# Kernel tuning notes

Measured on AMD Instinct MI355X. Metric: run time of the kernel, lower is better.

The kernel has to match this reference:

```python
import jax, jax.numpy as jnp
import numpy as np

LN_EPS = 1e-5


def setup_inputs() -> dict:
    key = jax.random.key(0)
    ks = jax.random.split(key, 4)
    B, D, N = 256, 1024, 100000
    scale = 1.0 / np.sqrt(D)
    return {
        "query": jax.random.normal(ks[0], (B, D), dtype=jnp.float32),
        "W1": jax.random.normal(ks[1], (D, D), dtype=jnp.float32) * scale,
        "b1": jnp.zeros((D,), dtype=jnp.float32),
        "ln_g": jnp.ones((D,), dtype=jnp.float32),
        "ln_b": jnp.zeros((D,), dtype=jnp.float32),
        "W2": jax.random.normal(ks[2], (D, D), dtype=jnp.float32) * scale,
        "b2": jnp.zeros((D,), dtype=jnp.float32),
        "memory": jax.random.normal(ks[3], (N, D), dtype=jnp.float32),
        "k": 16,
    }


def _l2norm(x):
    # F.normalize(p=2, dim=-1): x / max(||x||, eps) with eps=1e-12
    n = jnp.sqrt(jnp.sum(x * x, axis=-1, keepdims=True))
    return x / jnp.maximum(n, 1e-12)


def _layernorm(x, g, b):
    mu = jnp.mean(x, axis=-1, keepdims=True)
    var = jnp.mean((x - mu) ** 2, axis=-1, keepdims=True)
    return (x - mu) * jax.lax.rsqrt(var + LN_EPS) * g + b


def reference(query, W1, b1, ln_g, ln_b, W2, b2, memory, k):
    # project(): Linear -> LayerNorm -> GELU (exact) -> Linear -> L2 normalize
    h = query @ W1.T + b1                      # [B, D]
    h = _layernorm(h, ln_g, ln_b)
    h = jax.nn.gelu(h, approximate=False)
    refined = _l2norm(h @ W2.T + b2)           # [B, D]

    # retrieve_similar(): cosine sims against normalized memory bank, then top-k
    mem_n = _l2norm(memory)                    # [N, D]
    sims = refined @ mem_n.T                   # [B, N]
    topk_vals, topk_idx = jax.lax.top_k(sims, k)   # [B, k]
    retrieved = mem_n[topk_idx]                # [B, k, D] gather
    return refined, topk_vals, topk_idx, retrieved
```

## Files before the change

### kernel.cpp

```cpp
#include <hip/hip_runtime.h>
#include <float.h>
#include <math.h>

#define D 1024
#define BQ 256
#define NMEM 100000
#define TOPK 16
#define NT_TOT 1563

typedef __attribute__((ext_vector_type(4))) float f32x4;
typedef __attribute__((ext_vector_type(8))) short s16x8;

__device__ __forceinline__ void mfma16(f32x4& d, s16x8 a, s16x8 b) {
  asm("v_mfma_f32_16x16x32_bf16 %0, %1, %2, %0" : "+v"(d) : "v"(a), "v"(b));
}

typedef __attribute__((address_space(3))) unsigned int lds_u32_t;
typedef __attribute__((address_space(1))) const unsigned int gbl_u32_t;
__device__ __forceinline__ void async_copy16(const void* gsrc, void* ldst) {
  __builtin_amdgcn_global_load_lds((gbl_u32_t*)gsrc, (lds_u32_t*)ldst, 16, 0, 0);
}

#define GLOAD(dst, addr) \
  asm volatile("global_load_dwordx4 %0, %1, off" : "=v"(dst) : "v"(addr))

__device__ __forceinline__ unsigned short bf16rtne(float x) {
  unsigned u = __float_as_uint(x);
  unsigned r = u + 0x7fffu + ((u >> 16) & 1u);
  return (unsigned short)(r >> 16);
}

__device__ __forceinline__ void cvt8(f32x4 a, f32x4 b, s16x8* hi, s16x8* lo,
                                     float* ssq) {
  float xs[8] = {a[0], a[1], a[2], a[3], b[0], b[1], b[2], b[3]};
  union { s16x8 v; unsigned short u[8]; } H, L;
#pragma unroll
  for (int e = 0; e < 8; ++e) {
    float x = xs[e];
    unsigned short h = bf16rtne(x);
    float hf = __uint_as_float(((unsigned)h) << 16);
    H.u[e] = (short)h;
    L.u[e] = (short)bf16rtne(x - hf);
    *ssq = fmaf(x, x, *ssq);
  }
  *hi = H.v;
  *lo = L.v;
}


__device__ __forceinline__ float waveReduceSum(float v) {
#pragma unroll
  for (int o = 32; o > 0; o >>= 1) v += __shfl_xor(v, o, 64);
  return v;
}

__device__ __forceinline__ float blockReduceSum(float v, float* sbuf) {
  v = waveReduceSum(v);
  int w = threadIdx.x >> 6;
  if ((threadIdx.x & 63) == 0) sbuf[w] = v;
  __syncthreads();
  float r = sbuf[0] + sbuf[1] + sbuf[2] + sbuf[3];
  __syncthreads();
  return r;
}


__global__ __launch_bounds__(256) void prep_bf16_kernel(
    const float* __restrict__ src, float* __restrict__ dst, int R16) {
  int g = blockIdx.x * 256 + threadIdx.x;
  int l = g & 63;
  int mt = (g >> 6) % R16;
  int kb = (g >> 6) / R16;
  int row = mt * 16 + (l & 15);
  int k0 = kb * 32 + ((l >> 4) << 3);
  const float* s = src + (size_t)row * D + k0;
  float4 v0 = *(const float4*)s;
  float4 v1 = *(const float4*)(s + 4);
  float xs[8] = {v0.x, v0.y, v0.z, v0.w, v1.x, v1.y, v1.z, v1.w};
  union { uint4 q; unsigned short u[8]; } H, L;
#pragma unroll
  for (int e = 0; e < 8; ++e) {
    float x = xs[e];
    unsigned short h = bf16rtne(x);
    float hf = __uint_as_float(((unsigned)h) << 16);
    H.u[e] = h;
    L.u[e] = bf16rtne(x - hf);
  }
  char* db = (char*)dst + (size_t)kb * (R16 * 2048) + mt * 2048 + l * 16;
  *(uint4*)db = H.q;
  *(uint4*)(db + 1024) = L.q;
}


__global__ __launch_bounds__(256) void mfma_gemm_kernel(
    const float* __restrict__ Afr, const float* __restrict__ Wfr,
    float* __restrict__ part) {
  int t = threadIdx.x;
  int w = t >> 6, l = t & 63;
  int ct = blockIdx.x & 63;
  int kc = blockIdx.x >> 6;
  f32x4 acc[4];
  f32x4 zz = {0.f, 0.f, 0.f, 0.f};
#pragma unroll
  for (int mi = 0; mi < 4; ++mi) acc[mi] = zz;
  const char* ab0 = (const char*)Afr + w * 8192 + l * 16;
  const char* bb0 = (const char*)Wfr + ct * 2048 + l * 16;
#pragma unroll 2
  for (int s = 0; s < 8; ++s) {
    int kb = kc * 8 + s;
    const char* bb = bb0 + (size_t)kb * 131072;
    s16x8 bh = *(const s16x8*)(bb);
    s16x8 bl = *(const s16x8*)(bb + 1024);
    const char* ab = ab0 + (size_t)kb * 32768;
#pragma unroll
    for (int mi = 0; mi < 4; ++mi) {
      s16x8 ah = *(const s16x8*)(ab + mi * 2048);
      s16x8 al = *(const s16x8*)(ab + mi * 2048 + 1024);
      mfma16(acc[mi], ah, bh);
      mfma16(acc[mi], ah, bl);
      mfma16(acc[mi], al, bh);
    }
  }
  float* pb = part + (size_t)kc * 262144 + ct * 16 + (l & 15);
#pragma unroll
  for (int mi = 0; mi < 4; ++mi)
#pragma unroll
    for (int j = 0; j < 4; ++j) {
      int row = w * 64 + mi * 16 + ((l >> 4) << 2) + j;
      pb[(size_t)row * 1024] = acc[mi][j];
    }
}


__global__ __launch_bounds__(256) void reduce_ln_gelu_kernel(
    const float* __restrict__ part, const float* __restrict__ bias,
    const float* __restrict__ g, const float* __restrict__ b,
    float* __restrict__ Hf) {
  __shared__ float sbuf[4];
  int row = blockIdx.x, t = threadIdx.x;
  const float* p = part + (size_t)row * 1024 + t * 4;
  float4 x0 = *(const float4*)(p);
  float4 x1 = *(const float4*)(p + 262144);
  float4 x2 = *(const float4*)(p + 524288);
  float4 x3 = *(const float4*)(p + 786432);
  float4 bb = *(const float4*)(bias + t * 4);
  float vx = x0.x + x1.x + x2.x + x3.x + bb.x;
  float vy = x0.y + x1.y + x2.y + x3.y + bb.y;
  float vz = x0.z + x1.z + x2.z + x3.z + bb.z;
  float vw = x0.w + x1.w + x2.w + x3.w + bb.w;
  float s = blockReduceSum(vx + vy + vz + vw, sbuf);
  float mu = s * (1.0f / D);
  float dx = vx - mu, dy = vy - mu, dz = vz - mu, dw = vw - mu;
  float ss = blockReduceSum(dx * dx + dy * dy + dz * dz + dw * dw, sbuf);
  float rstd = rsqrtf(ss * (1.0f / D) + 1e-5f);
  float4 gg = *(const float4*)(g + t * 4);
  float4 be = *(const float4*)(b + t * 4);
  float y[4];
  y[0] = dx * rstd * gg.x + be.x;
  y[1] = dy * rstd * gg.y + be.y;
  y[2] = dz * rstd * gg.z + be.z;
  y[3] = dw * rstd * gg.w + be.w;
  const float c = 0.70710678118654752f;
  union { uint2 q; unsigned short u[4]; } H, L;
#pragma unroll
  for (int e = 0; e < 4; ++e) {
    float ye = 0.5f * y[e] * (1.0f + erff(y[e] * c));
    unsigned short h = bf16rtne(ye);
    float hf = __uint_as_float(((unsigned)h) << 16);
    H.u[e] = h;
    L.u[e] = bf16rtne(ye - hf);
  }
  int kb = t >> 3, oct = (t >> 1) & 3;
  char* db = (char*)Hf + (size_t)kb * 32768 + (row >> 4) * 2048 +
             ((row & 15) + oct * 16) * 16 + (t & 1) * 8;
  *(uint2*)db = H.q;
  *(uint2*)(db + 1024) = L.q;
}


__global__ __launch_bounds__(256) void reduce_l2norm_kernel(
    const float* __restrict__ part, const float* __restrict__ bias,
    float* __restrict__ outRef, float* __restrict__ Af) {
  __shared__ float sbuf[4];
  int row = blockIdx.x, t = threadIdx.x;
  const float* p = part + (size_t)row * 1024 + t * 4;
  float4 x0 = *(const float4*)(p);
  float4 x1 = *(const float4*)(p + 262144);
  float4 x2 = *(const float4*)(p + 524288);
  float4 x3 = *(const float4*)(p + 786432);
  float4 bb = *(const float4*)(bias + t * 4);
  float vx = x0.x + x1.x + x2.x + x3.x + bb.x;
  float vy = x0.y + x1.y + x2.y + x3.y + bb.y;
  float vz = x0.z + x1.z + x2.z + x3.z + bb.z;
  float vw = x0.w + x1.w + x2.w + x3.w + bb.w;
  float ss = blockReduceSum(vx * vx + vy * vy + vz * vz + vw * vw, sbuf);
  float inv = 1.0f / fmaxf(sqrtf(ss), 1e-12f);
  float y[4] = {vx * inv, vy * inv, vz * inv, vw * inv};
  *(float4*)(outRef + (size_t)row * D + t * 4) =
      make_float4(y[0], y[1], y[2], y[3]);
  union { uint2 q; unsigned short u[4]; } H, L;
#pragma unroll
  for (int e = 0; e < 4; ++e) {
    unsigned short h = bf16rtne(y[e]);
    float hf = __uint_as_float(((unsigned)h) << 16);
    H.u[e] = h;
    L.u[e] = bf16rtne(y[e] - hf);
  }
  int kb = t >> 3, oct = (t >> 1) & 3;
  char* db = (char*)Af + (size_t)kb * 32768 + (row >> 4) * 2048 +
             ((row & 15) + oct * 16) * 16 + (t & 1) * 8;
  *(uint2*)db = H.q;
  *(uint2*)(db + 1024) = L.q;
}

__global__ void zero_ctrs_kernel(int* c) { c[threadIdx.x] = 0; }


#define SBODY(J, CV0, CV1, NV0, NV1, PBR, PBW, DO_A, DO_PF, DO_CONV, VMC,      \
              DO_BAR2, VME)                                                    \
  do {                                                                         \
    _Pragma("unroll") for (int mi = 0; mi < 4; ++mi) {                         \
      const char* ab_ = smem + (w4 + mi) * 2048 + l * 16;                      \
      ah[mi] = *(const s16x8*)ab_;                                             \
      al[mi] = *(const s16x8*)(ab_ + 1024);                                    \
    }                                                                          \
    asm volatile("s_waitcnt lgkmcnt(0)\n\ts_barrier" ::: "memory");            \
    if (DO_A) {                                                                \
      const char* as_ =                                                        \
          afbytes + (size_t)((J) + 1) * 32768 + w * 8192 + l * 16;             \
      char* ad_ = smem + w * 8192;                                             \
      _Pragma("unroll") for (int u = 0; u < 8; ++u)                            \
        async_copy16(as_ + u * 1024, ad_ + u * 1024);                          \
    }                                                                          \
    if (DO_PF) {                                                               \
      const float* p_ = bsrc + ((J) + 2) * 32;                                 \
      GLOAD(NV0, p_);                                                          \
      GLOAD(NV1, p_ + 4);                                                      \
    }                                                                          \
    if (DO_CONV) {                                                             \
      asm volatile("s_waitcnt vmcnt(" #VMC ")" ::: "memory");                  \
      __builtin_amdgcn_sched_barrier(0);                                       \
      s16x8 bhn_, bln_;                                                        \
      cvt8(CV0, CV1, &bhn_, &bln_, &ssq);                                      \
      *(s16x8*)(smem + 32768 + (PBW)*8192 + bwoff) = bhn_;                     \
      *(s16x8*)(smem + 32768 + (PBW)*8192 + bwoff + 1024) = bln_;              \
    }                                                                          \
    __builtin_amdgcn_s_setprio(1);                                             \
    _Pragma("unroll") for (int ni = 0; ni < 4; ++ni) {                         \
      const char* bb_ = smem + 32768 + (PBR)*8192 + ni * 2048 + l * 16;        \
      s16x8 bh_ = *(const s16x8*)bb_;                                          \
      s16x8 bl_ = *(const s16x8*)(bb_ + 1024);                                 \
      _Pragma("unroll") for (int mi = 0; mi < 4; ++mi) {                       \
        mfma16(acc[mi][ni], ah[mi], bh_);                                      \
        mfma16(acc[mi][ni], ah[mi], bl_);                                      \
        mfma16(acc[mi][ni], al[mi], bh_);                                      \
      }                                                                        \
    }                                                                          \
    __builtin_amdgcn_s_setprio(0);                                             \
    if (DO_BAR2)                                                               \
      asm volatile("s_waitcnt vmcnt(" #VME ") lgkmcnt(0)\n\ts_barrier" :::     \
                       "memory");                                              \
  } while (0)

__global__ __launch_bounds__(256, 3) void sims_gemm_kernel(
    const float* __restrict__ Afrag, const float* __restrict__ mem,
    float* __restrict__ invn, int* __restrict__ ctr,
    float* __restrict__ simsbuf, int ntiles, int chunk_n0, int stride_cols) {
  __shared__ __align__(16) char smem[50432];
  __shared__ int s_tile;
  const int t = threadIdx.x;
  const int w = t >> 6, l = t & 63;
  const int w4 = w * 4;
  const int brow_loc = t >> 2;
  const int kseg = t & 3;
  const int bwoff = (brow_loc >> 4) * 2048 + ((brow_loc & 15) + kseg * 16) * 16;
  const char* afbytes = (const char*)Afrag;
  float* sPf = (float*)(smem + 49152);
  float* sInvF = (float*)(smem + 50176);

  while (true) {
    if (t == 0) s_tile = atomicAdd(ctr, 1);
    __syncthreads();
    const int unit = s_tile;
    if (unit >= ntiles) break;
    const int n0 = chunk_n0 + unit * 64;
    const int brow = min(n0 + brow_loc, NMEM - 1);
    const float* bsrc = mem + (size_t)brow * D + kseg * 8;

    f32x4 acc[4][4];
    f32x4 zz = {0.f, 0.f, 0.f, 0.f};
#pragma unroll
    for (int mi = 0; mi < 4; ++mi)
#pragma unroll
      for (int ni = 0; ni < 4; ++ni) acc[mi][ni] = zz;
    float ssq = 0.f;
    s16x8 ah[4], al[4];
    f32x4 br_a0, br_a1, br_b0, br_b1;

    GLOAD(br_a0, bsrc);
    GLOAD(br_a1, bsrc + 4);
    {
      const float* p1 = bsrc + 32;
      GLOAD(br_b0, p1);
      GLOAD(br_b1, p1 + 4);
    }
    {
      const char* as_ = afbytes + w * 8192 + l * 16;
      char* ad_ = smem + w * 8192;
#pragma unroll
      for (int u = 0; u < 8; ++u) async_copy16(as_ + u * 1024, ad_ + u * 1024);
    }
    asm volatile("s_waitcnt vmcnt(10)" ::: "memory");
    __builtin_amdgcn_sched_barrier(0);
    {
      s16x8 bh0, bl0;
      cvt8(br_a0, br_a1, &bh0, &bl0, &ssq);
      *(s16x8*)(smem + 32768 + bwoff) = bh0;
      *(s16x8*)(smem + 32768 + bwoff + 1024) = bl0;
    }
    asm volatile("s_waitcnt vmcnt(2) lgkmcnt(0)\n\ts_barrier" ::: "memory");

#pragma unroll 1
    for (int j = 0; j < 30; j += 2) {
      SBODY(j, br_b0, br_b1, br_a0, br_a1, 0, 1, 1, 1, 1, 10, 1, 2);
      SBODY(j + 1, br_a0, br_a1, br_b0, br_b1, 1, 0, 1, 1, 1, 10, 1, 2);
    }
    SBODY(30, br_b0, br_b1, br_a0, br_a1, 0, 1, 1, 0, 1, 8, 1, 0);
    SBODY(31, br_a0, br_a1, br_b0, br_b1, 1, 0, 0, 0, 0, 0, 0, 0);

    __syncthreads();
    sPf[t] = ssq;
    __syncthreads();
    if (t < 64) {
      float s = sPf[t * 4] + sPf[t * 4 + 1] + sPf[t * 4 + 2] + sPf[t * 4 + 3];
      float inv = 1.0f / fmaxf(sqrtf(s), 1e-12f);
      sInvF[t] = inv;
      int col = n0 + t;
      if (col < NMEM) invn[col] = inv;
    }
    __syncthreads();
    float siv[4];
#pragma unroll
    for (int ni = 0; ni < 4; ++ni) siv[ni] = sInvF[ni * 16 + (l & 15)];
    float* srow = simsbuf + (size_t)(unit * 64);
#pragma unroll
    for (int mi = 0; mi < 4; ++mi)
#pragma unroll
      for (int jj = 0; jj < 4; ++jj) {
        int row = w * 64 + mi * 16 + ((l >> 4) << 2) + jj;
        float* rp = srow + (size_t)row * stride_cols;
#pragma unroll
        for (int ni = 0; ni < 4; ++ni)
          rp[ni * 16 + (l & 15)] = acc[mi][ni][jj] * siv[ni];
      }
  }
}


__global__ __launch_bounds__(512) void topk_chunk_kernel(
    const float* __restrict__ simsbuf, int stride_cols, int chunk_n0,
    int nvalid, float* __restrict__ cv, int* __restrict__ ci) {
  __shared__ float wvv[8];
  __shared__ int wii[8];
  __shared__ float sbv;
  __shared__ int sbi;
  int row = blockIdx.x, t = threadIdx.x;
  const float* S = simsbuf + (size_t)row * stride_cols;
  float tv[16];
  int ti[16];
#pragma unroll
  for (int s = 0; s < 16; ++s) { tv[s] = -FLT_MAX; ti[s] = 2147483647; }
  float curMin = -FLT_MAX;
  for (int c0 = t * 4; c0 < nvalid; c0 += 2048) {
    float vv[4] = {-FLT_MAX, -FLT_MAX, -FLT_MAX, -FLT_MAX};
    if (c0 + 4 <= nvalid) {
      float4 v = *(const float4*)(S + c0);
      vv[0] = v.x; vv[1] = v.y; vv[2] = v.z; vv[3] = v.w;
    } else {
#pragma unroll
      for (int e = 0; e < 4; ++e)
        if (c0 + e < nvalid) vv[e] = S[c0 + e];
    }
#pragma unroll
    for (int e = 0; e < 4; ++e) {
      float v = vv[e];
      if (v > curMin) {
        int n = chunk_n0 + c0 + e;
        int ms = 0;
        float mv = tv[0];
#pragma unroll
        for (int s = 1; s < 16; ++s)
          if (tv[s] < mv) { mv = tv[s]; ms = s; }
#pragma unroll
        for (int s = 0; s < 16; ++s)
          if (s == ms) { tv[s] = v; ti[s] = n; }
        curMin = tv[0];
#pragma unroll
        for (int s = 1; s < 16; ++s) curMin = fminf(curMin, tv[s]);
      }
    }
  }
  float lastV = FLT_MAX;
  int lastI = -1;
  for (int pass = 0; pass < TOPK; ++pass) {
    float bv = -FLT_MAX;
    int bi = 2147483647;
#pragma unroll
    for (int s = 0; s < 16; ++s) {
      float v = tv[s];
      int idx = ti[s];
      bool qual = (v < lastV) || (v == lastV && idx > lastI);
      bool bet = (v > bv) || (v == bv && idx < bi);
      if (qual && bet) { bv = v; bi = idx; }
    }
#pragma unroll
    for (int o = 32; o > 0; o >>= 1) {
      float v2 = __shfl_xor(bv, o, 64);
      int i2 = __shfl_xor(bi, o, 64);
      if (v2 > bv || (v2 == bv && i2 < bi)) { bv = v2; bi = i2; }
    }
    if ((t & 63) == 0) { wvv[t >> 6] = bv; wii[t >> 6] = bi; }
    __syncthreads();
    if (t == 0) {
      float fv = wvv[0];
      int fi = wii[0];
#pragma unroll
      for (int u = 1; u < 8; ++u) {
        if (wvv[u] > fv || (wvv[u] == fv && wii[u] < fi)) {
          fv = wvv[u];
          fi = wii[u];
        }
      }
      sbv = fv;
      sbi = fi;
      cv[row * TOPK + pass] = fv;
      ci[row * TOPK + pass] = fi;
    }
    __syncthreads();
    lastV = sbv;
    lastI = sbi;
  }
}


__global__ __launch_bounds__(64) void final_merge_kernel(
    const float* __restrict__ cand_v, const int* __restrict__ cand_i,
    int nchunk, float* __restrict__ out_vals, float* __restrict__ out_idx) {
  int row = blockIdx.x, l = threadIdx.x;
  int nc = nchunk * TOPK;
  float mv[8];
  int mi_[8];
#pragma unroll
  for (int u = 0; u < 8; ++u) {
    int p = l + u * 64;
    if (p < nc) {
      int ch = p >> 4;
      mv[u] = cand_v[ch * 4096 + row * TOPK + (p & 15)];
      mi_[u] = cand_i[ch * 4096 + row * TOPK + (p & 15)];
    } else {
      mv[u] = -FLT_MAX;
      mi_[u] = 2147483647;
    }
  }
  float lastV = FLT_MAX;
  int lastI = -1;
  for (int pass = 0; pass < TOPK; ++pass) {
    float bv = -FLT_MAX;
    int bi = 2147483647;
#pragma unroll
    for (int u = 0; u < 8; ++u) {
      bool qual = (mv[u] < lastV) || (mv[u] == lastV && mi_[u] > lastI);
      bool bet = (mv[u] > bv) || (mv[u] == bv && mi_[u] < bi);
      if (qual && bet) { bv = mv[u]; bi = mi_[u]; }
    }
#pragma unroll
    for (int o = 32; o > 0; o >>= 1) {
      float v2 = __shfl_xor(bv, o, 64);
      int i2 = __shfl_xor(bi, o, 64);
      if (v2 > bv || (v2 == bv && i2 < bi)) { bv = v2; bi = i2; }
    }
    bv = __shfl(bv, 0, 64);
    bi = __shfl(bi, 0, 64);
    if (l == 0) {
      out_vals[row * TOPK + pass] = bv;
      out_idx[row * TOPK + pass] = (float)bi;
    }
    lastV = bv;
    lastI = bi;
  }
}


__global__ __launch_bounds__(256) void gather_kernel(
    const float* __restrict__ out_idx, const float* __restrict__ mem,
    const float* __restrict__ invn, float* __restrict__ out_retr) {
  int p = blockIdx.x;
  int idx = (int)out_idx[p];
  float inv = invn[idx];
  int c = threadIdx.x * 4;
  float4 v = *(const float4*)(mem + (size_t)idx * D + c);
  v.x *= inv; v.y *= inv; v.z *= inv; v.w *= inv;
  *(float4*)(out_retr + (size_t)p * D + c) = v;
}


extern "C" void kernel_launch(void* const* d_in, const int* in_sizes, int n_in,
                              void* d_out, int out_size, void* d_ws,
                              size_t ws_size, hipStream_t stream) {
  const float* query = (const float*)d_in[0];
  const float* W1 = (const float*)d_in[1];
  const float* b1 = (const float*)d_in[2];
  const float* ln_g = (const float*)d_in[3];
  const float* ln_b = (const float*)d_in[4];
  const float* W2 = (const float*)d_in[5];
  const float* b2 = (const float*)d_in[6];
  const float* mem = (const float*)d_in[7];

  float* out = (float*)d_out;
  float* out_refined = out;
  float* out_vals = out + 262144;
  float* out_idx = out + 262144 + 4096;
  float* out_retr = out + 262144 + 8192;

  float* wsp = (float*)d_ws;
  float* invn = wsp;
  float* Qf = wsp + 100352;
  float* Af = wsp + 362496;
  float* W1f = wsp + 624640;
  float* W2f = wsp + 1673216;
  float* part = wsp + 2721792;
  float* cand_v = wsp + 3770368;
  int* cand_i = (int*)(wsp + 3901440);
  int* ctrs = (int*)(wsp + 4032512);
  float* sims = wsp + 4032576;

  long ws_floats = (long)(ws_size / 4);
  long avail = ws_floats - 4032640;
  int tpc = (int)(avail / 16384);
  if (tpc > NT_TOT) tpc = NT_TOT;
  if (tpc < 1) tpc = 1;
  int nchunk = (NT_TOT + tpc - 1) / tpc;
  if (nchunk > 32) nchunk = 32;
  tpc = (NT_TOT + nchunk - 1) / nchunk;
  int stride = tpc * 64;

  zero_ctrs_kernel<<<1, 64, 0, stream>>>(ctrs);
  prep_bf16_kernel<<<128, 256, 0, stream>>>(query, Qf, 16);
  prep_bf16_kernel<<<512, 256, 0, stream>>>(W1, W1f, 64);
  prep_bf16_kernel<<<512, 256, 0, stream>>>(W2, W2f, 64);
  mfma_gemm_kernel<<<256, 256, 0, stream>>>(Qf, W1f, part);
  reduce_ln_gelu_kernel<<<256, 256, 0, stream>>>(part, b1, ln_g, ln_b, Qf);
  mfma_gemm_kernel<<<256, 256, 0, stream>>>(Qf, W2f, part);
  reduce_l2norm_kernel<<<256, 256, 0, stream>>>(part, b2, out_refined, Af);
  for (int c = 0; c < nchunk; ++c) {
    int t0 = c * tpc;
    int nt = NT_TOT - t0;
    if (nt > tpc) nt = tpc;
    if (nt <= 0) break;
    int base = t0 * 64;
    sims_gemm_kernel<<<768, 256, 0, stream>>>(Af, mem, invn, ctrs + c, sims,
                                              nt, base, stride);
    int nvalid = NMEM - base;
    if (nvalid > nt * 64) nvalid = nt * 64;
    topk_chunk_kernel<<<256, 512, 0, stream>>>(sims, stride, base, nvalid,
                                               cand_v + c * 4096,
                                               cand_i + c * 4096);
  }
  final_merge_kernel<<<256, 64, 0, stream>>>(cand_v, cand_i, nchunk, out_vals,
                                             out_idx);
  gather_kernel<<<BQ * TOPK, 256, 0, stream>>>(out_idx, mem, invn, out_retr);
}
```

Measured before the change: 419.7 us.

## Load A fragments directly to registers and triple-buffer B prefetch in sims GEMM

```diff
diff --git a/kernel.cpp b/kernel.cpp
--- a/kernel.cpp
+++ b/kernel.cpp
@@ -15,24 +15,15 @@
   asm("v_mfma_f32_16x16x32_bf16 %0, %1, %2, %0" : "+v"(d) : "v"(a), "v"(b));
 }
 
-typedef __attribute__((address_space(3))) unsigned int lds_u32_t;
-typedef __attribute__((address_space(1))) const unsigned int gbl_u32_t;
-__device__ __forceinline__ void async_copy16(const void* gsrc, void* ldst) {
-  __builtin_amdgcn_global_load_lds((gbl_u32_t*)gsrc, (lds_u32_t*)ldst, 16, 0, 0);
-}
-
-#define GLOAD(dst, addr) \
-  asm volatile("global_load_dwordx4 %0, %1, off" : "=v"(dst) : "v"(addr))
-
 __device__ __forceinline__ unsigned short bf16rtne(float x) {
   unsigned u = __float_as_uint(x);
   unsigned r = u + 0x7fffu + ((u >> 16) & 1u);
   return (unsigned short)(r >> 16);
 }
 
-__device__ __forceinline__ void cvt8(f32x4 a, f32x4 b, s16x8* hi, s16x8* lo,
+__device__ __forceinline__ void cvt8(float4 a, float4 b, s16x8* hi, s16x8* lo,
                                      float* ssq) {
-  float xs[8] = {a[0], a[1], a[2], a[3], b[0], b[1], b[2], b[3]};
+  float xs[8] = {a.x, a.y, a.z, a.w, b.x, b.y, b.z, b.w};
   union { s16x8 v; unsigned short u[8]; } H, L;
 #pragma unroll
   for (int e = 0; e < 8; ++e) {
@@ -216,72 +207,64 @@
 __global__ void zero_ctrs_kernel(int* c) { c[threadIdx.x] = 0; }
 
 
-#define SBODY(J, CV0, CV1, NV0, NV1, PBR, PBW, DO_A, DO_PF, DO_CONV, VMC,      \
-              DO_BAR2, VME)                                                    \
+#define SBODY(J, BP, ACh, ACl, ANh, ANl, RC0, RC1, RP0, RP1, DOPFB, DOPFA,    \
+              DOCONV)                                                          \
   do {                                                                         \
-    _Pragma("unroll") for (int mi = 0; mi < 4; ++mi) {                         \
-      const char* ab_ = smem + (w4 + mi) * 2048 + l * 16;                      \
-      ah[mi] = *(const s16x8*)ab_;                                             \
-      al[mi] = *(const s16x8*)(ab_ + 1024);                                    \
+    if (DOCONV) {                                                              \
+      s16x8 bhn_, bln_;                                                        \
+      cvt8(RC0, RC1, &bhn_, &bln_, &ssq);                                      \
+      char* bw_ = smem + (1 - (BP)) * 8192 + bwoff;                            \
+      *(s16x8*)bw_ = bhn_;                                                     \
+      *(s16x8*)(bw_ + 1024) = bln_;                                            \
     }                                                                          \
-    asm volatile("s_waitcnt lgkmcnt(0)\n\ts_barrier" ::: "memory");            \
-    if (DO_A) {                                                                \
-      const char* as_ =                                                        \
-          afbytes + (size_t)((J) + 1) * 32768 + w * 8192 + l * 16;             \
-      char* ad_ = smem + w * 8192;                                             \
-      _Pragma("unroll") for (int u = 0; u < 8; ++u)                            \
-        async_copy16(as_ + u * 1024, ad_ + u * 1024);                          \
+    if (DOPFA) {                                                               \
+      const char* an_ = afbytes + (size_t)((J) + 1) * 32768 + w4x + l * 16;    \
+      _Pragma("unroll") for (int mi = 0; mi < 4; ++mi) {                       \
+        ANh[mi] = *(const s16x8*)(an_ + mi * 2048);                            \
+        ANl[mi] = *(const s16x8*)(an_ + mi * 2048 + 1024);                     \
+      }                                                                        \
     }                                                                          \
-    if (DO_PF) {                                                               \
-      const float* p_ = bsrc + ((J) + 2) * 32;                                 \
-      GLOAD(NV0, p_);                                                          \
-      GLOAD(NV1, p_ + 4);                                                      \
-    }                                                                          \
-    if (DO_CONV) {                                                             \
-      asm volatile("s_waitcnt vmcnt(" #VMC ")" ::: "memory");                  \
-      __builtin_amdgcn_sched_barrier(0);                                       \
-      s16x8 bhn_, bln_;                                                        \
-      cvt8(CV0, CV1, &bhn_, &bln_, &ssq);                                      \
-      *(s16x8*)(smem + 32768 + (PBW)*8192 + bwoff) = bhn_;                     \
-      *(s16x8*)(smem + 32768 + (PBW)*8192 + bwoff + 1024) = bln_;              \
+    if (DOPFB) {                                                               \
+      const float* p_ = bsrc + ((J) + 3) * 32;                                 \
+      RP0 = *(const float4*)p_;                                                \
+      RP1 = *(const float4*)(p_ + 4);                                          \
     }                                                                          \
     __builtin_amdgcn_s_setprio(1);                                             \
     _Pragma("unroll") for (int ni = 0; ni < 4; ++ni) {                         \
-      const char* bb_ = smem + 32768 + (PBR)*8192 + ni * 2048 + l * 16;        \
+      const char* bb_ = smem + (BP)*8192 + ni * 2048 + l * 16;                 \
       s16x8 bh_ = *(const s16x8*)bb_;                                          \
       s16x8 bl_ = *(const s16x8*)(bb_ + 1024);                                 \
       _Pragma("unroll") for (int mi = 0; mi < 4; ++mi) {                       \
-        mfma16(acc[mi][ni], ah[mi], bh_);                                      \
-        mfma16(acc[mi][ni], ah[mi], bl_);                                      \
-        mfma16(acc[mi][ni], al[mi], bh_);                                      \
+        mfma16(acc[mi][ni], ACh[mi], bh_);                                     \
+        mfma16(acc[mi][ni], ACh[mi], bl_);                                     \
+        mfma16(acc[mi][ni], ACl[mi], bh_);                                     \
       }                                                                        \
     }                                                                          \
     __builtin_amdgcn_s_setprio(0);                                             \
-    if (DO_BAR2)                                                               \
-      asm volatile("s_waitcnt vmcnt(" #VME ") lgkmcnt(0)\n\ts_barrier" :::     \
-                       "memory");                                              \
+    asm volatile("s_waitcnt lgkmcnt(0)\n\ts_barrier" ::: "memory");            \
+    __builtin_amdgcn_sched_barrier(0);                                         \
   } while (0)
 
-__global__ __launch_bounds__(256, 3) void sims_gemm_kernel(
+__global__ __launch_bounds__(256, 2) void sims_gemm_kernel(
     const float* __restrict__ Afrag, const float* __restrict__ mem,
     float* __restrict__ invn, int* __restrict__ ctr,
     float* __restrict__ simsbuf, int ntiles, int chunk_n0, int stride_cols) {
-  __shared__ __align__(16) char smem[50432];
+  __shared__ __align__(16) char smem[16384];
+  __shared__ float sInvF[64];
   __shared__ int s_tile;
   const int t = threadIdx.x;
   const int w = t >> 6, l = t & 63;
-  const int w4 = w * 4;
+  const int w4x = (w * 4) * 2048;
   const int brow_loc = t >> 2;
   const int kseg = t & 3;
   const int bwoff = (brow_loc >> 4) * 2048 + ((brow_loc & 15) + kseg * 16) * 16;
   const char* afbytes = (const char*)Afrag;
-  float* sPf = (float*)(smem + 49152);
-  float* sInvF = (float*)(smem + 50176);
 
   while (true) {
     if (t == 0) s_tile = atomicAdd(ctr, 1);
     __syncthreads();
     const int unit = s_tile;
+    __syncthreads();
     if (unit >= ntiles) break;
     const int n0 = chunk_n0 + unit * 64;
     const int brow = min(n0 + brow_loc, NMEM - 1);
@@ -294,48 +277,57 @@
 #pragma unroll
       for (int ni = 0; ni < 4; ++ni) acc[mi][ni] = zz;
     float ssq = 0.f;
-    s16x8 ah[4], al[4];
-    f32x4 br_a0, br_a1, br_b0, br_b1;
-
-    GLOAD(br_a0, bsrc);
-    GLOAD(br_a1, bsrc + 4);
+
+    float4 r0a, r0b, r1a, r1b, r2a, r2b;
+    s16x8 s0h[4], s0l[4], s1h[4], s1l[4];
+
+    r0a = *(const float4*)bsrc;
+    r0b = *(const float4*)(bsrc + 4);
+    r1a = *(const float4*)(bsrc + 32);
+    r1b = *(const float4*)(bsrc + 36);
+    r2a = *(const float4*)(bsrc + 64);
+    r2b = *(const float4*)(bsrc + 68);
     {
-      const float* p1 = bsrc + 32;
-      GLOAD(br_b0, p1);
-      GLOAD(br_b1, p1 + 4);
-    }
-    {
-      const char* as_ = afbytes + w * 8192 + l * 16;
-      char* ad_ = smem + w * 8192;
-#pragma unroll
-      for (int u = 0; u < 8; ++u) async_copy16(as_ + u * 1024, ad_ + u * 1024);
-    }
-    asm volatile("s_waitcnt vmcnt(10)" ::: "memory");
-    __builtin_amdgcn_sched_barrier(0);
+      const char* a0_ = afbytes + w4x + l * 16;
+#pragma unroll
+      for (int mi = 0; mi < 4; ++mi) {
+        s0h[mi] = *(const s16x8*)(a0_ + mi * 2048);
+        s0l[mi] = *(const s16x8*)(a0_ + mi * 2048 + 1024);
+      }
+    }
     {
       s16x8 bh0, bl0;
-      cvt8(br_a0, br_a1, &bh0, &bl0, &ssq);
-      *(s16x8*)(smem + 32768 + bwoff) = bh0;
-      *(s16x8*)(smem + 32768 + bwoff + 1024) = bl0;
-    }
-    asm volatile("s_waitcnt vmcnt(2) lgkmcnt(0)\n\ts_barrier" ::: "memory");
+      cvt8(r0a, r0b, &bh0, &bl0, &ssq);
+      *(s16x8*)(smem + bwoff) = bh0;
+      *(s16x8*)(smem + bwoff + 1024) = bl0;
+    }
+    asm volatile("s_waitcnt lgkmcnt(0)\n\ts_barrier" ::: "memory");
+    __builtin_amdgcn_sched_barrier(0);
 
 #pragma unroll 1
-    for (int j = 0; j < 30; j += 2) {
-      SBODY(j, br_b0, br_b1, br_a0, br_a1, 0, 1, 1, 1, 1, 10, 1, 2);
-      SBODY(j + 1, br_a0, br_a1, br_b0, br_b1, 1, 0, 1, 1, 1, 10, 1, 2);
-    }
-    SBODY(30, br_b0, br_b1, br_a0, br_a1, 0, 1, 1, 0, 1, 8, 1, 0);
-    SBODY(31, br_a0, br_a1, br_b0, br_b1, 1, 0, 0, 0, 0, 0, 0, 0);
-
-    __syncthreads();
-    sPf[t] = ssq;
-    __syncthreads();
-    if (t < 64) {
-      float s = sPf[t * 4] + sPf[t * 4 + 1] + sPf[t * 4 + 2] + sPf[t * 4 + 3];
-      float inv = 1.0f / fmaxf(sqrtf(s), 1e-12f);
-      sInvF[t] = inv;
-      int col = n0 + t;
+    for (int jb = 0; jb < 24; jb += 6) {
+      SBODY(jb + 0, 0, s0h, s0l, s1h, s1l, r1a, r1b, r0a, r0b, 1, 1, 1);
+      SBODY(jb + 1, 1, s1h, s1l, s0h, s0l, r2a, r2b, r1a, r1b, 1, 1, 1);
+      SBODY(jb + 2, 0, s0h, s0l, s1h, s1l, r0a, r0b, r2a, r2b, 1, 1, 1);
+      SBODY(jb + 3, 1, s1h, s1l, s0h, s0l, r1a, r1b, r0a, r0b, 1, 1, 1);
+      SBODY(jb + 4, 0, s0h, s0l, s1h, s1l, r2a, r2b, r1a, r1b, 1, 1, 1);
+      SBODY(jb + 5, 1, s1h, s1l, s0h, s0l, r0a, r0b, r2a, r2b, 1, 1, 1);
+    }
+    SBODY(24, 0, s0h, s0l, s1h, s1l, r1a, r1b, r0a, r0b, 1, 1, 1);
+    SBODY(25, 1, s1h, s1l, s0h, s0l, r2a, r2b, r1a, r1b, 1, 1, 1);
+    SBODY(26, 0, s0h, s0l, s1h, s1l, r0a, r0b, r2a, r2b, 1, 1, 1);
+    SBODY(27, 1, s1h, s1l, s0h, s0l, r1a, r1b, r0a, r0b, 1, 1, 1);
+    SBODY(28, 0, s0h, s0l, s1h, s1l, r2a, r2b, r1a, r1b, 1, 1, 1);
+    SBODY(29, 1, s1h, s1l, s0h, s0l, r0a, r0b, r2a, r2b, 0, 1, 1);
+    SBODY(30, 0, s0h, s0l, s1h, s1l, r1a, r1b, r0a, r0b, 0, 1, 1);
+    SBODY(31, 1, s1h, s1l, s0h, s0l, r2a, r2b, r1a, r1b, 0, 0, 0);
+
+    float s2 = ssq + __shfl_xor(ssq, 1, 64);
+    s2 = s2 + __shfl_xor(s2, 2, 64);
+    float inv = 1.0f / fmaxf(sqrtf(s2), 1e-12f);
+    if (kseg == 0) {
+      sInvF[brow_loc] = inv;
+      int col = n0 + brow_loc;
       if (col < NMEM) invn[col] = inv;
     }
     __syncthreads();
@@ -353,6 +345,7 @@
         for (int ni = 0; ni < 4; ++ni)
           rp[ni * 16 + (l & 15)] = acc[mi][ni][jj] * siv[ni];
       }
+    __syncthreads();
   }
 }
 
@@ -558,7 +551,7 @@
     if (nt > tpc) nt = tpc;
     if (nt <= 0) break;
     int base = t0 * 64;
-    sims_gemm_kernel<<<768, 256, 0, stream>>>(Af, mem, invn, ctrs + c, sims,
+    sims_gemm_kernel<<<512, 256, 0, stream>>>(Af, mem, invn, ctrs + c, sims,
                                               nt, base, stride);
     int nvalid = NMEM - base;
     if (nvalid > nt * 64) nvalid = nt * 64;
```

After: 414.4 us. Within noise of the previous version (-1.3%).
